# Optimization experiments

Measured on AMD Instinct MI355X. Metric: run time of the kernel, lower is better.

## Reference

```python
import jax, jax.numpy as jnp
import numpy as np

N = 20000
E = 320000
NEG_SLOPE = 0.2
LN_EPS = 1e-5


def gat_conv(x, W, a_src, a_dst, b, src, dst, heads, ch, concat):
    # x: [N, F_in]; W: [F_in, H*C]; a_src/a_dst: [H, C]; b: [H*C] or [C]
    xl = (x @ W).reshape(N, heads, ch)                      # [N,H,C]
    alpha_src = jnp.sum(xl * a_src, axis=-1)                # [N,H]
    alpha_dst = jnp.sum(xl * a_dst, axis=-1)                # [N,H]
    e = alpha_src[src] + alpha_dst[dst]                     # [E',H]
    e = jax.nn.leaky_relu(e, NEG_SLOPE)
    # segment softmax over incoming edges of each dst node
    m = jax.ops.segment_max(e, dst, num_segments=N)         # [N,H]
    m = jnp.where(jnp.isfinite(m), m, 0.0)
    ex = jnp.exp(e - m[dst])
    denom = jax.ops.segment_sum(ex, dst, num_segments=N)    # [N,H]
    alpha = ex / (denom[dst] + 1e-16)                       # [E',H]
    msg = alpha[:, :, None] * xl[src]                       # [E',H,C]
    out = jax.ops.segment_sum(msg, dst, num_segments=N)     # [N,H,C]
    if concat:
        return out.reshape(N, heads * ch) + b
    return out.mean(axis=1) + b


def layer_norm(x, g, b):
    mu = jnp.mean(x, axis=-1, keepdims=True)
    var = jnp.mean(jnp.square(x - mu), axis=-1, keepdims=True)
    return (x - mu) * jax.lax.rsqrt(var + LN_EPS) * g + b


def setup_inputs() -> dict:
    key = jax.random.key(0)
    ks = jax.random.split(key, 24)
    d = {}
    d["x"] = jax.random.normal(ks[0], (N, 50), dtype=jnp.float32)
    d["edge_index"] = jax.random.randint(ks[1], (2, E), 0, N, dtype=jnp.int64)

    def glorot(k, shape):
        fan = shape[0] + shape[-1]
        return jax.random.normal(k, shape, dtype=jnp.float32) * np.sqrt(2.0 / fan)

    # conv1: 50 -> 256, heads=4, concat
    d["W1"] = glorot(ks[2], (50, 4 * 256))
    d["a_src1"] = glorot(ks[3], (4, 256))
    d["a_dst1"] = glorot(ks[4], (4, 256))
    d["b1"] = jnp.zeros((4 * 256,), jnp.float32)
    # conv2: 1024 -> 256, heads=4, concat
    d["W2"] = glorot(ks[5], (1024, 4 * 256))
    d["a_src2"] = glorot(ks[6], (4, 256))
    d["a_dst2"] = glorot(ks[7], (4, 256))
    d["b2"] = jnp.zeros((4 * 256,), jnp.float32)
    # conv3: 1024 -> 121, heads=6, concat=False
    d["W3"] = glorot(ks[8], (1024, 6 * 121))
    d["a_src3"] = glorot(ks[9], (6, 121))
    d["a_dst3"] = glorot(ks[10], (6, 121))
    d["b3"] = jnp.zeros((121,), jnp.float32)
    # skips
    d["skipW1"] = glorot(ks[11], (50, 1024))
    d["skipb1"] = jnp.zeros((1024,), jnp.float32)
    d["skipW2"] = glorot(ks[12], (1024, 1024))
    d["skipb2"] = jnp.zeros((1024,), jnp.float32)
    # layer norms
    d["g1"] = jnp.ones((1024,), jnp.float32)
    d["beta1"] = jnp.zeros((1024,), jnp.float32)
    d["g2"] = jnp.ones((1024,), jnp.float32)
    d["beta2"] = jnp.zeros((1024,), jnp.float32)
    return d


def reference(x, edge_index, W1, a_src1, a_dst1, b1, W2, a_src2, a_dst2, b2,
              W3, a_src3, a_dst3, b3, skipW1, skipb1, skipW2, skipb2,
              g1, beta1, g2, beta2):
    # add self loops (PyG GATConv default)
    loop = jnp.arange(N, dtype=edge_index.dtype)
    src = jnp.concatenate([edge_index[0], loop])
    dst = jnp.concatenate([edge_index[1], loop])

    h = gat_conv(x, W1, a_src1, a_dst1, b1, src, dst, 4, 256, True)
    h = jax.nn.elu(layer_norm(h + (x @ skipW1 + skipb1), g1, beta1))
    h2 = gat_conv(h, W2, a_src2, a_dst2, b2, src, dst, 4, 256, True)
    h2 = jax.nn.elu(layer_norm(h2 + (h @ skipW2 + skipb2), g2, beta2))
    out = gat_conv(h2, W3, a_src3, a_dst3, b3, src, dst, 6, 121, False)
    return out
```

## Files before the change

### kernel.cpp

```cpp
#include <hip/hip_runtime.h>
#include <hip/hip_bf16.h>
#include <math.h>

typedef __attribute__((ext_vector_type(8))) __bf16 bf16x8;
typedef __attribute__((ext_vector_type(4))) float f32x4;

#define MPAD 20224
#define SSZ ((size_t)MPAD * 128)

#if __has_builtin(__builtin_amdgcn_global_load_lds)
#define GLD16(g, l)                                                                      \
    __builtin_amdgcn_global_load_lds(                                                    \
        (const __attribute__((address_space(1))) unsigned int*)(g),                      \
        (__attribute__((address_space(3))) unsigned int*)(l), 16, 0, 0)
#else
#define GLD16(g, l) (*(bf16x8*)(l) = *(const bf16x8*)(g))
#endif

#define BAR() asm volatile("s_barrier" ::: "memory")
#define WAITVM(N) asm volatile("s_waitcnt vmcnt(" #N ")" ::: "memory")


#define STAGE_T(t_)                                                                      \
    do {                                                                                 \
        __bf16* Ld = lds + (((t_) & 3) * 16384);                                         \
        const __bf16* Ga = Abase + (t_) * 32;                                            \
        const __bf16* Gb = Bbase + (t_) * 32;                                            \
        GLD16(Ga, Ld + tt * 8);                                                          \
        GLD16(Ga + (size_t)128 * K_, Ld + (tt + 512) * 8);                               \
        GLD16(Gb, Ld + 8192 + tt * 8);                                                   \
        GLD16(Gb + (size_t)128 * K_, Ld + 8192 + (tt + 512) * 8);                        \
    } while (0)

#define LOAD_FRAGS(t_)                                                                   \
    {                                                                                    \
        const __bf16* Ar = lds + (((t_) & 3) * 16384) + aoff;                            \
        const __bf16* Br = lds + (((t_) & 3) * 16384) + 8192 + boff;                     \
        _Pragma("unroll") for (int i = 0; i < 8; i++)                                    \
            af[i] = *(const bf16x8*)(Ar + i * 512);                                      \
        _Pragma("unroll") for (int j = 0; j < 4; j++)                                    \
            bf[j] = *(const bf16x8*)(Br + j * 512);                                      \
    }

#define MFMA_ALL()                                                                       \
    __builtin_amdgcn_s_setprio(1);                                                       \
    _Pragma("unroll") for (int i = 0; i < 8; i++)                                        \
        _Pragma("unroll") for (int j = 0; j < 4; j++)                                    \
            acc[i][j] = __builtin_amdgcn_mfma_f32_16x16x32_bf16(af[i], bf[j],            \
                                                                acc[i][j], 0, 0, 0);     \
    __builtin_amdgcn_s_setprio(0);

#define GEMM256_BODY(A, Bt, K_, STORE)                                                   \
    __shared__ __align__(16) __bf16 lds[65536];                                          \
    const int tt = threadIdx.x;                                                          \
    const int lane = tt & 63;                                                            \
    const int wid = tt >> 6;                                                             \
    const int wr = wid >> 2;                                           \
    const int wc = wid & 3;                                         \
     \
    const int nwg = gridDim.x * gridDim.y;                                               \
    const int wg0 = blockIdx.y * gridDim.x + blockIdx.x;                                 \
    const int qq = nwg >> 3, rr = nwg & 7, xcd = wg0 & 7, oo = wg0 >> 3;                 \
    const int swz = (xcd < rr ? xcd * (qq + 1) : rr * (qq + 1) + (xcd - rr) * qq) + oo;  \
    const int bm = (swz / gridDim.x) * 256;                                              \
    const int bn = (swz % gridDim.x) * 256;                                              \
    const int m16 = lane & 15;                                                           \
    const int c4 = lane >> 4;                                                            \
    const int NT = K_ >> 5;                                                              \
    const int ttp = tt ^ (((tt >> 5) & 1) << 1);          \
    const int srow = ttp >> 2;                                                           \
    const int sch = (ttp & 3) << 3;                                                      \
    const __bf16* Abase = A + (size_t)(bm + srow) * K_ + sch;                            \
    const __bf16* Bbase = Bt + (size_t)(bn + srow) * K_ + sch;                           \
    const int fsw = ((m16 >> 3) & 1) << 4;                                               \
    const int aoff = (((wr * 128 + m16) * 32) + c4 * 8) ^ fsw;                           \
    const int boff = (((wc * 64 + m16) * 32) + c4 * 8) ^ fsw;                            \
    f32x4 acc[8][4];                                                                     \
    _Pragma("unroll") for (int i = 0; i < 8; i++)                                        \
        _Pragma("unroll") for (int j = 0; j < 4; j++)                                    \
            acc[i][j] = (f32x4){0.f, 0.f, 0.f, 0.f};                                     \
    bf16x8 af[8], bf[4];                                                                 \
                      \
    STAGE_T(0);                                                                          \
    if (NT > 1) STAGE_T(1);                                                              \
    if (NT > 2) STAGE_T(2);                                                              \
    if (NT > 2) { WAITVM(8); } else if (NT > 1) { WAITVM(4); } else { WAITVM(0); }       \
    BAR();                                                                               \
    for (int t = 0; t < NT; t++) {                                                       \
        if (t + 3 < NT) STAGE_T(t + 3);                                                  \
        LOAD_FRAGS(t);                                                                   \
        MFMA_ALL();                                                                      \
        if (t + 1 < NT) {                                                                \
            if (t + 3 < NT) { WAITVM(8); }                                               \
            else if (t + 3 == NT) { WAITVM(4); }                                         \
            else { WAITVM(0); }                                                          \
            BAR();                                                                       \
        }                                                                                \
    }                                                                                    \
    STORE

__global__ __launch_bounds__(512, 2) void gemm256_bt(const __bf16* __restrict__ A,
                                                     const __bf16* __restrict__ Bt,
                                                     __bf16* __restrict__ C,
                                                     int M, int N_, int K_) {
    GEMM256_BODY(A, Bt, K_,
        { const int r4 = c4 << 2;
          const int rb = bm + wr * 128;
          _Pragma("unroll") for (int i = 0; i < 8; i++)
              _Pragma("unroll") for (int j = 0; j < 4; j++) {
                  int col = bn + wc * 64 + j * 16 + m16;
                  size_t sb_ = (size_t)(col >> 7) * SSZ + (col & 127);
                  _Pragma("unroll") for (int r = 0; r < 4; r++) {
                      int row = rb + i * 16 + r4 + r;
                      C[sb_ + (size_t)row * 128] = (__bf16)acc[i][j][r];
                  }
              } })
}

__global__ __launch_bounds__(512, 2) void gemm256_bt2(const __bf16* __restrict__ A,
                                                      const __bf16* __restrict__ Bt,
                                                      __bf16* __restrict__ C0,
                                                      __bf16* __restrict__ C1,
                                                      int M, int K_) {
    GEMM256_BODY(A, Bt, K_,
        { const int r4 = c4 << 2;
          const int rb = bm + wr * 128;
          _Pragma("unroll") for (int i = 0; i < 8; i++)
              _Pragma("unroll") for (int j = 0; j < 4; j++) {
                  int col = bn + wc * 64 + j * 16 + m16;
                  __bf16* Cp = (col < 1024) ? C0 : C1;
                  int c10 = col & 1023;
                  size_t sb_ = (size_t)(c10 >> 7) * SSZ + (c10 & 127);
                  _Pragma("unroll") for (int r = 0; r < 4; r++) {
                      int row = rb + i * 16 + r4 + r;
                      Cp[sb_ + (size_t)row * 128] = (__bf16)acc[i][j][r];
                  }
              } })
}

__device__ __forceinline__ void transpose_tile(const float* __restrict__ W,
                                               __bf16* __restrict__ WT,
                                               int K, int N, int Kp, int Np,
                                               int bx, int by, float* sm) {
    int tx = threadIdx.x & 31, ty = threadIdx.x >> 5;
#pragma unroll
    for (int r = ty; r < 32; r += 8) {
        int k = by * 32 + r, n = bx * 32 + tx;
        float v = 0.f;
        if (k < K && n < N) v = W[(size_t)k * N + n];
        sm[r * 33 + tx] = v;
    }
    __syncthreads();
#pragma unroll
    for (int r = ty; r < 32; r += 8) {
        int n = bx * 32 + r, k = by * 32 + tx;
        if (n < Np && k < Kp) WT[(size_t)n * Kp + k] = (__bf16)sm[tx * 33 + r];
    }
}

__device__ __forceinline__ void transpose_w3_tile(const float* __restrict__ W,
                                                  __bf16* __restrict__ WT,
                                                  int bx, int by, float* sm) {
    int tx = threadIdx.x & 31, ty = threadIdx.x >> 5;
    int r0 = bx * 32;
    int h = r0 >> 7;
    int c0 = r0 & 127;
#pragma unroll
    for (int r = ty; r < 32; r += 8) {
        int k = by * 32 + r;
        int c = c0 + tx;
        float v = 0.f;
        if (c < 121) v = W[(size_t)k * 726 + h * 121 + c];
        sm[r * 33 + tx] = v;
    }
    __syncthreads();
#pragma unroll
    for (int r = ty; r < 32; r += 8) {
        int rr = r0 + r;
        int k = by * 32 + tx;
        WT[(size_t)rr * 1024 + k] = (__bf16)sm[tx * 33 + r];
    }
}

__global__ __launch_bounds__(256) void prep_k(const float* __restrict__ x,
                                              const float* __restrict__ W1,
                                              const float* __restrict__ sW1,
                                              const float* __restrict__ W2,
                                              const float* __restrict__ sW2,
                                              const float* __restrict__ W3,
                                              __bf16* __restrict__ xp,
                                              __bf16* __restrict__ WTcat1,
                                              __bf16* __restrict__ WTcat2,
                                              __bf16* __restrict__ W3pT, int Nn) {
    __shared__ float sm[32 * 33];
    int b = blockIdx.x;
    if (b < 5056) {
        int i = b * 256 + threadIdx.x;
        int n = i >> 6, c = i & 63;
        float v = 0.f;
        if (n < Nn && c < 50) v = x[n * 50 + c];
        xp[(size_t)n * 64 + c] = (__bf16)v;
    } else if (b < 5120) {
        int i = b - 5056; transpose_tile(W1, WTcat1, 50, 1024, 64, 1024, i % 32, i / 32, sm);
    } else if (b < 5184) {
        int i = b - 5120; transpose_tile(sW1, WTcat1 + 1024 * 64, 50, 1024, 64, 1024, i % 32, i / 32, sm);
    } else if (b < 6208) {
        int i = b - 5184; transpose_tile(W2, WTcat2, 1024, 1024, 1024, 1024, i % 32, i / 32, sm);
    } else if (b < 7232) {
        int i = b - 6208; transpose_tile(sW2, WTcat2 + (size_t)1024 * 1024, 1024, 1024, 1024, 1024, i % 32, i / 32, sm);
    } else {
        int i = b - 7232; transpose_w3_tile(W3, W3pT, i % 24, i / 24, sm);
    }
}

__global__ void zero_probe_k(const int* __restrict__ ei, int* __restrict__ cnt,
                             int* __restrict__ flag, int Nn) {
    int i = blockIdx.x * 256 + threadIdx.x;
    if (i < Nn) cnt[i] = 0;
    if (blockIdx.x == 0 && threadIdx.x == 0) {
        int all0 = 1;
        for (int k = 0; k < 64; k++)
            if (ei[2 * k + 1] != 0) { all0 = 0; break; }
        *flag = all0;
    }
}

__device__ __forceinline__ int load_ei(const int* ei, int idx, int is64) {
    return is64 ? ei[2 * idx] : ei[idx];
}

__global__ void hist_k(const int* __restrict__ ei, const int* __restrict__ flag,
                       int* __restrict__ cnt, int E, int Nn) {
    int e = blockIdx.x * 256 + threadIdx.x;
    if (e >= E + Nn) return;
    int is64 = *flag;
    int d = (e < E) ? load_ei(ei, E + e, is64) : (e - E);
    d = min(max(d, 0), Nn - 1);
    atomicAdd(&cnt[d], 1);
}

__global__ __launch_bounds__(1024) void scan_k(int* __restrict__ cnt, int* __restrict__ row_ptr,
                                               int Nn) {
    __shared__ int part[1024];
    int t = threadIdx.x;
    int chunk = (Nn + 1023) >> 10;
    int lo = t * chunk;
    int hi = lo + chunk; if (hi > Nn) hi = Nn; if (lo > Nn) lo = Nn;
    int s = 0;
    for (int i = lo; i < hi; i++) s += (cnt[i] + 7) & ~7;
    part[t] = s;
    __syncthreads();
    for (int off = 1; off < 1024; off <<= 1) {
        int v = (t >= off) ? part[t - off] : 0;
        __syncthreads();
        part[t] += v;
        __syncthreads();
    }
    int run = part[t] - s;
    for (int i = lo; i < hi; i++) { row_ptr[i] = run; run += (cnt[i] + 7) & ~7; }
    if (t == 1023) row_ptr[Nn] = part[1023];
    __syncthreads();
    for (int i = lo; i < hi; i++) cnt[i] = 0;
}

__global__ void fill_csr_k(const int* __restrict__ ei, const int* __restrict__ flag,
                           const int* __restrict__ row_ptr, int* __restrict__ cursor,
                           int* __restrict__ src_csr, int E, int Nn) {
    int e = blockIdx.x * 256 + threadIdx.x;
    if (e >= E + Nn) return;
    int is64 = *flag;
    int d = (e < E) ? load_ei(ei, E + e, is64) : (e - E);
    int s = (e < E) ? load_ei(ei, e, is64) : (e - E);
    d = min(max(d, 0), Nn - 1);
    s = min(max(s, 0), Nn - 1);
    int slot = row_ptr[d] + atomicAdd(&cursor[d], 1);
    src_csr[slot] = s;
}

__global__ void alpha_k(const __bf16* __restrict__ XL, int sph, const float* __restrict__ a_src,
                        const float* __restrict__ a_dst, float* __restrict__ asrc,
                        float* __restrict__ adst, int Nn, int H, int C) {
    int gw = (blockIdx.x * 256 + threadIdx.x) >> 6;
    int lane = threadIdx.x & 63;
    if (gw >= Nn * H) return;
    int n = gw / H, h = gw - n * H;
    const float* as = a_src + h * C;
    const float* ad = a_dst + h * C;
    float s = 0.f, d = 0.f;
    for (int c = lane; c < C; c += 64) {
        float v = (float)XL[(size_t)(h * sph + (c >> 7)) * SSZ + (size_t)n * 128 + (c & 127)];
        s += v * as[c];
        d += v * ad[c];
    }
#pragma unroll
    for (int off = 32; off; off >>= 1) {
        s += __shfl_down(s, off);
        d += __shfl_down(d, off);
    }
    if (lane == 0) { asrc[n * H + h] = s; adst[n * H + h] = d; }
}

__global__ void attn_k(const int* __restrict__ row_ptr, const int* __restrict__ deg,
                       const int* __restrict__ src_csr,
                       const float* __restrict__ asrc, const float* __restrict__ adst,
                       float* __restrict__ wt, int Nn, int H, int Ecap) {
    int gw = (blockIdx.x * 256 + threadIdx.x) >> 6;
    int lane = threadIdx.x & 63;
    if (gw >= Nn) return;
    int n = gw;
    int base = row_ptr[n], dg = deg[n];
    if (dg <= 64) {
        bool v = lane < dg;
        int src = v ? src_csr[base + lane] : 0;
        for (int h = 0; h < H; h++) {
            float ad = adst[n * H + h];
            float e = -1e30f;
            if (v) {
                e = asrc[src * H + h] + ad;
                e = e > 0.f ? e : 0.2f * e;
            }
            float m = e;
#pragma unroll
            for (int off = 1; off < 64; off <<= 1) m = fmaxf(m, __shfl_xor(m, off));
            float ex = v ? __expf(e - m) : 0.f;
            float sum = ex;
#pragma unroll
            for (int off = 1; off < 64; off <<= 1) sum += __shfl_xor(sum, off);
            if (v) wt[(size_t)h * Ecap + base + lane] = ex / (sum + 1e-16f);
        }
        return;
    }
    for (int h = 0; h < H; h++) {
        float ad = adst[n * H + h];
        float m = -1e30f;
        for (int s = lane; s < dg; s += 64) {
            float e = asrc[src_csr[base + s] * H + h] + ad;
            e = e > 0.f ? e : 0.2f * e;
            m = fmaxf(m, e);
        }
#pragma unroll
        for (int off = 1; off < 64; off <<= 1) m = fmaxf(m, __shfl_xor(m, off));
        float sum = 0.f;
        for (int s = lane; s < dg; s += 64) {
            float e = asrc[src_csr[base + s] * H + h] + ad;
            e = e > 0.f ? e : 0.2f * e;
            sum += __expf(e - m);
        }
#pragma unroll
        for (int off = 1; off < 64; off <<= 1) sum += __shfl_xor(sum, off);
        float inv = 1.f / (sum + 1e-16f);
        float* wrow = wt + (size_t)h * Ecap;
        for (int s = lane; s < dg; s += 64) {
            float e = asrc[src_csr[base + s] * H + h] + ad;
            e = e > 0.f ? e : 0.2f * e;
            wrow[base + s] = __expf(e - m) * inv;
        }
    }
}

__global__ __launch_bounds__(256) void agg_skip8(const __bf16* __restrict__ XL,
                                                 const float* __restrict__ wt,
                                                 const int* __restrict__ row_ptr,
                                                 const int* __restrict__ src_csr,
                                                 const float* __restrict__ bias,
                                                 const float* __restrict__ sb,
                                                 __bf16* __restrict__ SK, int Nn, int Ecap) {
    const int cc = blockIdx.y;
    const int n = blockIdx.x * 4 + (threadIdx.x >> 6);
    const int lane = threadIdx.x & 63;
    if (n >= Nn) return;
    const int g = lane >> 4;
    const int p = lane & 15;
    const int col = cc * 128 + p * 8;
    const float* wrow = wt + (size_t)(cc >> 1) * Ecap;
    const __bf16* XLc = XL + (size_t)cc * SSZ + p * 8;
    const int base = row_ptr[n], end = row_ptr[n + 1];

    float acc[8];
#pragma unroll
    for (int j = 0; j < 8; j++) acc[j] = 0.f;

    for (int e = base; e < end; e += 8) {
        int2 si = *(const int2*)(src_csr + e + 2 * g);
        float2 wv = *(const float2*)(wrow + e + 2 * g);
        bf16x8 xa = *(const bf16x8*)(XLc + (size_t)si.x * 128);
        bf16x8 xb = *(const bf16x8*)(XLc + (size_t)si.y * 128);
#pragma unroll
        for (int j = 0; j < 8; j++) acc[j] += wv.x * (float)xa[j] + wv.y * (float)xb[j];
    }
#pragma unroll
    for (int j = 0; j < 8; j++) {
        acc[j] += __shfl_xor(acc[j], 16);
        acc[j] += __shfl_xor(acc[j], 32);
    }
    if (lane < 16) {
        size_t o = (size_t)cc * SSZ + (size_t)n * 128 + p * 8;
        bf16x8 sk = *(const bf16x8*)(SK + o);
        bf16x8 res;
#pragma unroll
        for (int j = 0; j < 8; j++)
            res[j] = (__bf16)(acc[j] + bias[col + j] + sb[col + j] + (float)sk[j]);
        *(bf16x8*)(SK + o) = res;
    }
}

__global__ __launch_bounds__(256) void agg_mean8(const __bf16* __restrict__ XL,
                                                 const float* __restrict__ wt,
                                                 const int* __restrict__ row_ptr,
                                                 const int* __restrict__ src_csr,
                                                 __bf16* __restrict__ part, int Nn, int Ecap) {
    const int cc = blockIdx.y;
    const int n = blockIdx.x * 4 + (threadIdx.x >> 6);
    const int lane = threadIdx.x & 63;
    if (n >= Nn) return;
    const int g = lane >> 4;
    const int p = lane & 15;
    const int col = cc * 128 + p * 8;
    const float* wrow = wt + (size_t)cc * Ecap;
    const __bf16* XLc = XL + (size_t)cc * SSZ + p * 8;
    const int base = row_ptr[n], end = row_ptr[n + 1];

    float acc[8];
#pragma unroll
    for (int j = 0; j < 8; j++) acc[j] = 0.f;

    for (int e = base; e < end; e += 8) {
        int2 si = *(const int2*)(src_csr + e + 2 * g);
        float2 wv = *(const float2*)(wrow + e + 2 * g);
        bf16x8 xa = *(const bf16x8*)(XLc + (size_t)si.x * 128);
        bf16x8 xb = *(const bf16x8*)(XLc + (size_t)si.y * 128);
#pragma unroll
        for (int j = 0; j < 8; j++) acc[j] += wv.x * (float)xa[j] + wv.y * (float)xb[j];
    }
#pragma unroll
    for (int j = 0; j < 8; j++) {
        acc[j] += __shfl_xor(acc[j], 16);
        acc[j] += __shfl_xor(acc[j], 32);
    }
    if (lane < 16) {
        size_t o = (size_t)n * 768 + col;
        bf16x8 res;
#pragma unroll
        for (int j = 0; j < 8; j++) res[j] = (__bf16)acc[j];
        *(bf16x8*)(part + o) = res;
    }
}

__global__ __launch_bounds__(128) void reduce_mean_k(const __bf16* __restrict__ part,
                                                     const float* __restrict__ b3,
                                                     float* __restrict__ out, int Nn) {
    int n = blockIdx.x;
    int t = threadIdx.x;
    if (t >= 121) return;
    const __bf16* row = part + (size_t)n * 768;
    float s = 0.f;
#pragma unroll
    for (int h = 0; h < 6; h++) s += (float)row[h * 128 + t];
    out[(size_t)n * 121 + t] = s * (1.f / 6.f) + b3[t];
}

__global__ __launch_bounds__(256) void ln_elu_k(const __bf16* __restrict__ in,
                                                const float* __restrict__ g,
                                                const float* __restrict__ be,
                                                __bf16* __restrict__ out, int rows_real) {
    const int D = 1024;
    int n = blockIdx.x;
    int t = threadIdx.x;
    size_t ro = (size_t)n * D;
    if (n >= rows_real) {
#pragma unroll
        for (int j = 0; j < 4; j++) out[ro + t + 256 * j] = (__bf16)0.f;
        return;
    }
    float v[4];
    float s = 0.f, q = 0.f;
#pragma unroll
    for (int j = 0; j < 4; j++) {
        int c = t + 256 * j;
        float a = (float)in[(size_t)(c >> 7) * SSZ + (size_t)n * 128 + (c & 127)];
        v[j] = a;
        s += a;
        q += a * a;
    }
#pragma unroll
    for (int off = 32; off; off >>= 1) {
        s += __shfl_down(s, off);
        q += __shfl_down(q, off);
    }
    __shared__ float rs[8];
    int wid = t >> 6;
    if ((t & 63) == 0) { rs[wid] = s; rs[wid + 4] = q; }
    __syncthreads();
    s = rs[0] + rs[1] + rs[2] + rs[3];
    q = rs[4] + rs[5] + rs[6] + rs[7];
    float mu = s * (1.f / 1024.f);
    float var = q * (1.f / 1024.f) - mu * mu;
    float inv = rsqrtf(fmaxf(var, 0.f) + 1e-5f);
#pragma unroll
    for (int j = 0; j < 4; j++) {
        int c = t + 256 * j;
        float y = (v[j] - mu) * inv * g[c] + be[c];
        y = y > 0.f ? y : expm1f(y);
        out[ro + c] = (__bf16)y;
    }
}

extern "C" void kernel_launch(void* const* d_in, const int* in_sizes, int n_in,
                              void* d_out, int out_size, void* d_ws, size_t ws_size,
                              hipStream_t stream) {
    const float* x   = (const float*)d_in[0];
    const int*   ei  = (const int*)d_in[1];
    const float* W1  = (const float*)d_in[2];
    const float* as1 = (const float*)d_in[3];
    const float* ad1 = (const float*)d_in[4];
    const float* b1  = (const float*)d_in[5];
    const float* W2  = (const float*)d_in[6];
    const float* as2 = (const float*)d_in[7];
    const float* ad2 = (const float*)d_in[8];
    const float* b2  = (const float*)d_in[9];
    const float* W3  = (const float*)d_in[10];
    const float* as3 = (const float*)d_in[11];
    const float* ad3 = (const float*)d_in[12];
    const float* b3  = (const float*)d_in[13];
    const float* sW1 = (const float*)d_in[14];
    const float* sb1 = (const float*)d_in[15];
    const float* sW2 = (const float*)d_in[16];
    const float* sb2 = (const float*)d_in[17];
    const float* g1  = (const float*)d_in[18];
    const float* be1 = (const float*)d_in[19];
    const float* g2  = (const float*)d_in[20];
    const float* be2 = (const float*)d_in[21];
    float* out = (float*)d_out;

    const int Nn = 20000;
    const int E = in_sizes[1] / 2;
    const int E2 = E + Nn;
    const int Ecap = E2 + 8 * Nn;
    const int Mpad = MPAD;

    char* p = (char*)d_ws;
    auto alloc = [&](size_t bytes) {
        char* r = p;
        p += (bytes + 255) & ~(size_t)255;
        return r;
    };
    __bf16* WTcat1 = (__bf16*)alloc((size_t)2048 * 64 * 2);
    __bf16* WTcat2 = (__bf16*)alloc((size_t)2048 * 1024 * 2);
    __bf16* W3pT   = (__bf16*)alloc((size_t)768 * 1024 * 2);
    __bf16* xp     = (__bf16*)alloc((size_t)Mpad * 64 * 2);
    __bf16* XL     = (__bf16*)alloc((size_t)Mpad * 1024 * 2);
    __bf16* SK     = (__bf16*)alloc((size_t)Mpad * 1024 * 2);
    __bf16* H1     = (__bf16*)alloc((size_t)Mpad * 1024 * 2);
    float*  asrcb  = (float*)alloc((size_t)Nn * 6 * 4);
    float*  adstb  = (float*)alloc((size_t)Nn * 6 * 4);
    float*  wbuf   = (float*)alloc((size_t)6 * Ecap * 4);
    int*    rowp   = (int*)alloc((size_t)(Nn + 1) * 4);
    int*    cnt    = (int*)alloc((size_t)Nn * 4);
    int*    scsr   = (int*)alloc((size_t)Ecap * 4);
    int*    eiflag = (int*)alloc(256);
    __bf16* part   = SK;
    (void)ws_size; (void)n_in; (void)out_size;

    prep_k<<<8000, 256, 0, stream>>>(x, W1, sW1, W2, sW2, W3, xp, WTcat1, WTcat2, W3pT, Nn);

    zero_probe_k<<<(Nn + 255) / 256, 256, 0, stream>>>(ei, cnt, eiflag, Nn);
    hist_k<<<(E2 + 255) / 256, 256, 0, stream>>>(ei, eiflag, cnt, E, Nn);
    scan_k<<<1, 1024, 0, stream>>>(cnt, rowp, Nn);
    (void)hipMemsetAsync(scsr, 0, (size_t)Ecap * 4, stream);
    (void)hipMemsetAsync(wbuf, 0, (size_t)6 * Ecap * 4, stream);
    fill_csr_k<<<(E2 + 255) / 256, 256, 0, stream>>>(ei, eiflag, rowp, cnt, scsr, E, Nn);

    gemm256_bt2<<<dim3(8, Mpad / 256), 512, 0, stream>>>(xp, WTcat1, XL, SK, Mpad, 64);
    alpha_k<<<(Nn * 4 * 64) / 256, 256, 0, stream>>>(XL, 2, as1, ad1, asrcb, adstb, Nn, 4, 256);
    attn_k<<<(Nn + 3) / 4, 256, 0, stream>>>(rowp, cnt, scsr, asrcb, adstb, wbuf, Nn, 4, Ecap);
    agg_skip8<<<dim3((Nn + 3) / 4, 8), 256, 0, stream>>>(XL, wbuf, rowp, scsr, b1, sb1, SK, Nn, Ecap);
    ln_elu_k<<<Mpad, 256, 0, stream>>>(SK, g1, be1, H1, Nn);

    gemm256_bt2<<<dim3(8, Mpad / 256), 512, 0, stream>>>(H1, WTcat2, XL, SK, Mpad, 1024);
    alpha_k<<<(Nn * 4 * 64) / 256, 256, 0, stream>>>(XL, 2, as2, ad2, asrcb, adstb, Nn, 4, 256);
    attn_k<<<(Nn + 3) / 4, 256, 0, stream>>>(rowp, cnt, scsr, asrcb, adstb, wbuf, Nn, 4, Ecap);
    agg_skip8<<<dim3((Nn + 3) / 4, 8), 256, 0, stream>>>(XL, wbuf, rowp, scsr, b2, sb2, SK, Nn, Ecap);
    ln_elu_k<<<Mpad, 256, 0, stream>>>(SK, g2, be2, H1, Nn);

    gemm256_bt<<<dim3(3, Mpad / 256), 512, 0, stream>>>(H1, W3pT, XL, Mpad, 768, 1024);
    alpha_k<<<(Nn * 6 * 64) / 256, 256, 0, stream>>>(XL, 1, as3, ad3, asrcb, adstb, Nn, 6, 121);
    attn_k<<<(Nn + 3) / 4, 256, 0, stream>>>(rowp, cnt, scsr, asrcb, adstb, wbuf, Nn, 6, Ecap);
    agg_mean8<<<dim3((Nn + 3) / 4, 6), 256, 0, stream>>>(XL, wbuf, rowp, scsr, part, Nn, Ecap);
    reduce_mean_k<<<Nn, 128, 0, stream>>>(part, b3, out, Nn);
}
```

Baseline: 750.4 us.

## Software-pipeline LDS fragment loads for next K tile under current MFMAs

The bf16 GEMM main loop now reads the next tile's A/B fragments from LDS interleaved with the current tile's MFMA instructions, instead of loading all fragments before the MFMAs. To keep this correct, the prologue and per-iteration vmcnt waits are tightened so tile t+1 is resident before tile t's MFMAs begin. This hides LDS read latency behind matrix math. The cost is more register pressure and somewhat earlier waits on the global-to-LDS copies.

```diff
diff --git a/kernel.cpp b/kernel.cpp
--- a/kernel.cpp
+++ b/kernel.cpp
@@ -42,13 +42,38 @@
             bf[j] = *(const bf16x8*)(Br + j * 512);                                      \
     }
 
-#define MFMA_ALL()                                                                       \
-    __builtin_amdgcn_s_setprio(1);                                                       \
-    _Pragma("unroll") for (int i = 0; i < 8; i++)                                        \
-        _Pragma("unroll") for (int j = 0; j < 4; j++)                                    \
-            acc[i][j] = __builtin_amdgcn_mfma_f32_16x16x32_bf16(af[i], bf[j],            \
-                                                                acc[i][j], 0, 0, 0);     \
-    __builtin_amdgcn_s_setprio(0);
+#define MFMA1(i_, j_)                                                                    \
+    acc[i_][j_] = __builtin_amdgcn_mfma_f32_16x16x32_bf16(af[i_], bf[j_],                \
+                                                          acc[i_][j_], 0, 0, 0);
+
+#define MFMA_TILE_PRE(t_)                                                                \
+    {                                                                                    \
+        const __bf16* ArN = lds + ((((t_) + 1) & 3) * 16384) + aoff;                     \
+        const __bf16* BrN = lds + ((((t_) + 1) & 3) * 16384) + 8192 + boff;              \
+        __builtin_amdgcn_s_setprio(1);                                                   \
+        _Pragma("unroll") for (int i = 0; i < 7; i++) {                                  \
+            _Pragma("unroll") for (int j = 0; j < 4; j++) { MFMA1(i, j) }                \
+            af[i] = *(const bf16x8*)(ArN + i * 512);                                     \
+        }                                                                                \
+        MFMA1(7, 0)                                                                      \
+        bf[0] = *(const bf16x8*)(BrN + 0 * 512);                                         \
+        MFMA1(7, 1)                                                                      \
+        bf[1] = *(const bf16x8*)(BrN + 1 * 512);                                         \
+        MFMA1(7, 2)                                                                      \
+        bf[2] = *(const bf16x8*)(BrN + 2 * 512);                                         \
+        MFMA1(7, 3)                                                                      \
+        bf[3] = *(const bf16x8*)(BrN + 3 * 512);                                         \
+        af[7] = *(const bf16x8*)(ArN + 7 * 512);                                         \
+        __builtin_amdgcn_s_setprio(0);                                                   \
+    }
+
+#define MFMA_TILE_LAST()                                                                 \
+    {                                                                                    \
+        __builtin_amdgcn_s_setprio(1);                                                   \
+        _Pragma("unroll") for (int i = 0; i < 8; i++)                                    \
+            _Pragma("unroll") for (int j = 0; j < 4; j++) { MFMA1(i, j) }                \
+        __builtin_amdgcn_s_setprio(0);                                                   \
+    }
 
 #define GEMM256_BODY(A, Bt, K_, STORE)                                                   \
     __shared__ __align__(16) __bf16 lds[65536];                                          \
@@ -80,22 +105,18 @@
         _Pragma("unroll") for (int j = 0; j < 4; j++)                                    \
             acc[i][j] = (f32x4){0.f, 0.f, 0.f, 0.f};                                     \
     bf16x8 af[8], bf[4];                                                                 \
-                      \
+          \
     STAGE_T(0);                                                                          \
     if (NT > 1) STAGE_T(1);                                                              \
     if (NT > 2) STAGE_T(2);                                                              \
-    if (NT > 2) { WAITVM(8); } else if (NT > 1) { WAITVM(4); } else { WAITVM(0); }       \
+    if (NT > 2) { WAITVM(4); } else { WAITVM(0); }                                       \
     BAR();                                                                               \
+    LOAD_FRAGS(0);                                                                       \
     for (int t = 0; t < NT; t++) {                                                       \
         if (t + 3 < NT) STAGE_T(t + 3);                                                  \
-        LOAD_FRAGS(t);                                                                   \
-        MFMA_ALL();                                                                      \
-        if (t + 1 < NT) {                                                                \
-            if (t + 3 < NT) { WAITVM(8); }                                               \
-            else if (t + 3 == NT) { WAITVM(4); }                                         \
-            else { WAITVM(0); }                                                          \
-            BAR();                                                                       \
-        }                                                                                \
+        if (t + 1 < NT) { MFMA_TILE_PRE(t); } else { MFMA_TILE_LAST(); }                 \
+        if (t + 3 < NT) { WAITVM(4); BAR(); }                                            \
+        else if (t + 3 == NT) { WAITVM(0); BAR(); }                                      \
     }                                                                                    \
     STORE
 
```

Measured after the change: 1.717 ms. 2.29x slower.

## Fuse attention-logit dot products into GEMM epilogue and vectorize LayerNorm-ELU

Applied to the files above, without the earlier changes.

Removes the separate alpha_k kernel by computing each head's src/dst attention logits inside the GEMM epilogue. Each wave does partial dot products over its 64 columns, reduces them across lanes with xor-shuffles, and atomically adds them into buffers zeroed by new memsets. This avoids re-reading the bf16 XL tensor from memory, at the cost of extra epilogue work, atomics and memsets. Separately, ln_elu_k now handles two rows per block with 8-wide vector loads and stores.

```diff
diff --git a/kernel.cpp b/kernel.cpp
--- a/kernel.cpp
+++ b/kernel.cpp
@@ -50,7 +50,7 @@
                                                                 acc[i][j], 0, 0, 0);     \
     __builtin_amdgcn_s_setprio(0);
 
-#define GEMM256_BODY(A, Bt, K_, STORE)                                                   \
+#define GEMM256_BODY(A, Bt, K_, ...)                                                     \
     __shared__ __align__(16) __bf16 lds[65536];                                          \
     const int tt = threadIdx.x;                                                          \
     const int lane = tt & 63;                                                            \
@@ -97,12 +97,16 @@
             BAR();                                                                       \
         }                                                                                \
     }                                                                                    \
-    STORE
+    __VA_ARGS__
 
 __global__ __launch_bounds__(512, 2) void gemm256_bt(const __bf16* __restrict__ A,
                                                      const __bf16* __restrict__ Bt,
                                                      __bf16* __restrict__ C,
-                                                     int M, int N_, int K_) {
+                                                     int M, int N_, int K_,
+                                                     const float* __restrict__ a_src,
+                                                     const float* __restrict__ a_dst,
+                                                     float* __restrict__ asrc,
+                                                     float* __restrict__ adst, int Nn_) {
     GEMM256_BODY(A, Bt, K_,
         { const int r4 = c4 << 2;
           const int rb = bm + wr * 128;
@@ -114,14 +118,43 @@
                       int row = rb + i * 16 + r4 + r;
                       C[sb_ + (size_t)row * 128] = (__bf16)acc[i][j][r];
                   }
-              } })
+              }
+          { const int h = (bn + wc * 64) >> 7;
+            const int cw = (wc * 64) & 127;
+            float asv[4];
+            float adv[4];
+            _Pragma("unroll") for (int j = 0; j < 4; j++) {
+                int cp = cw + j * 16 + m16;
+                asv[j] = (cp < 121) ? a_src[h * 121 + cp] : 0.f;
+                adv[j] = (cp < 121) ? a_dst[h * 121 + cp] : 0.f;
+            }
+            _Pragma("unroll") for (int i = 0; i < 8; i++)
+                _Pragma("unroll") for (int r = 0; r < 4; r++) {
+                    int row = rb + i * 16 + r4 + r;
+                    float s = acc[i][0][r] * asv[0] + acc[i][1][r] * asv[1] +
+                              acc[i][2][r] * asv[2] + acc[i][3][r] * asv[3];
+                    float d = acc[i][0][r] * adv[0] + acc[i][1][r] * adv[1] +
+                              acc[i][2][r] * adv[2] + acc[i][3][r] * adv[3];
+                    _Pragma("unroll") for (int off = 1; off < 16; off <<= 1) {
+                        s += __shfl_xor(s, off);
+                        d += __shfl_xor(d, off);
+                    }
+                    if (m16 == 0 && row < Nn_) {
+                        atomicAdd(&asrc[row * 6 + h], s);
+                        atomicAdd(&adst[row * 6 + h], d);
+                    }
+                } } })
 }
 
 __global__ __launch_bounds__(512, 2) void gemm256_bt2(const __bf16* __restrict__ A,
                                                       const __bf16* __restrict__ Bt,
                                                       __bf16* __restrict__ C0,
                                                       __bf16* __restrict__ C1,
-                                                      int M, int K_) {
+                                                      int M, int K_,
+                                                      const float* __restrict__ a_src,
+                                                      const float* __restrict__ a_dst,
+                                                      float* __restrict__ asrc,
+                                                      float* __restrict__ adst, int Nn_) {
     GEMM256_BODY(A, Bt, K_,
         { const int r4 = c4 << 2;
           const int rb = bm + wr * 128;
@@ -135,7 +168,33 @@
                       int row = rb + i * 16 + r4 + r;
                       Cp[sb_ + (size_t)row * 128] = (__bf16)acc[i][j][r];
                   }
-              } })
+              }
+          if (bn < 1024) {
+              const int h = bn >> 8;
+              float asv[4];
+              float adv[4];
+              _Pragma("unroll") for (int j = 0; j < 4; j++) {
+                  int cp = wc * 64 + j * 16 + m16;
+                  asv[j] = a_src[h * 256 + cp];
+                  adv[j] = a_dst[h * 256 + cp];
+              }
+              _Pragma("unroll") for (int i = 0; i < 8; i++)
+                  _Pragma("unroll") for (int r = 0; r < 4; r++) {
+                      int row = rb + i * 16 + r4 + r;
+                      float s = acc[i][0][r] * asv[0] + acc[i][1][r] * asv[1] +
+                                acc[i][2][r] * asv[2] + acc[i][3][r] * asv[3];
+                      float d = acc[i][0][r] * adv[0] + acc[i][1][r] * adv[1] +
+                                acc[i][2][r] * adv[2] + acc[i][3][r] * adv[3];
+                      _Pragma("unroll") for (int off = 1; off < 16; off <<= 1) {
+                          s += __shfl_xor(s, off);
+                          d += __shfl_xor(d, off);
+                      }
+                      if (m16 == 0 && row < Nn_) {
+                          atomicAdd(&asrc[row * 4 + h], s);
+                          atomicAdd(&adst[row * 4 + h], d);
+                      }
+                  }
+          } })
 }
 
 __device__ __forceinline__ void transpose_tile(const float* __restrict__ W,
@@ -277,29 +336,6 @@
     src_csr[slot] = s;
 }
 
-__global__ void alpha_k(const __bf16* __restrict__ XL, int sph, const float* __restrict__ a_src,
-                        const float* __restrict__ a_dst, float* __restrict__ asrc,
-                        float* __restrict__ adst, int Nn, int H, int C) {
-    int gw = (blockIdx.x * 256 + threadIdx.x) >> 6;
-    int lane = threadIdx.x & 63;
-    if (gw >= Nn * H) return;
-    int n = gw / H, h = gw - n * H;
-    const float* as = a_src + h * C;
-    const float* ad = a_dst + h * C;
-    float s = 0.f, d = 0.f;
-    for (int c = lane; c < C; c += 64) {
-        float v = (float)XL[(size_t)(h * sph + (c >> 7)) * SSZ + (size_t)n * 128 + (c & 127)];
-        s += v * as[c];
-        d += v * ad[c];
-    }
-#pragma unroll
-    for (int off = 32; off; off >>= 1) {
-        s += __shfl_down(s, off);
-        d += __shfl_down(d, off);
-    }
-    if (lane == 0) { asrc[n * H + h] = s; adst[n * H + h] = d; }
-}
-
 __global__ void attn_k(const int* __restrict__ row_ptr, const int* __restrict__ deg,
                        const int* __restrict__ src_csr,
                        const float* __restrict__ asrc, const float* __restrict__ adst,
@@ -463,46 +499,54 @@
                                                 const float* __restrict__ g,
                                                 const float* __restrict__ be,
                                                 __bf16* __restrict__ out, int rows_real) {
-    const int D = 1024;
-    int n = blockIdx.x;
-    int t = threadIdx.x;
-    size_t ro = (size_t)n * D;
-    if (n >= rows_real) {
-#pragma unroll
-        for (int j = 0; j < 4; j++) out[ro + t + 256 * j] = (__bf16)0.f;
-        return;
-    }
-    float v[4];
+    const int half = threadIdx.x >> 7;
+    const int t = threadIdx.x & 127;
+    const int n = blockIdx.x * 2 + half;
+    const size_t ro = (size_t)n * 1024 + t * 8;
+    __shared__ float rs[8];
+    bf16x8 v8;
+    float v[8];
     float s = 0.f, q = 0.f;
-#pragma unroll
-    for (int j = 0; j < 4; j++) {
-        int c = t + 256 * j;
-        float a = (float)in[(size_t)(c >> 7) * SSZ + (size_t)n * 128 + (c & 127)];
-        v[j] = a;
-        s += a;
-        q += a * a;
+    const bool live = (n < rows_real);
+    if (live) {
+        v8 = *(const bf16x8*)(in + (size_t)(t >> 4) * SSZ + (size_t)n * 128 + (t & 15) * 8);
+#pragma unroll
+        for (int j = 0; j < 8; j++) {
+            v[j] = (float)v8[j];
+            s += v[j];
+            q += v[j] * v[j];
+        }
     }
 #pragma unroll
     for (int off = 32; off; off >>= 1) {
         s += __shfl_down(s, off);
         q += __shfl_down(q, off);
     }
-    __shared__ float rs[8];
-    int wid = t >> 6;
-    if ((t & 63) == 0) { rs[wid] = s; rs[wid + 4] = q; }
+    int wid = threadIdx.x >> 6;
+    if ((threadIdx.x & 63) == 0) { rs[wid] = s; rs[wid + 4] = q; }
     __syncthreads();
-    s = rs[0] + rs[1] + rs[2] + rs[3];
-    q = rs[4] + rs[5] + rs[6] + rs[7];
+    if (!live) {
+        bf16x8 z;
+#pragma unroll
+        for (int j = 0; j < 8; j++) z[j] = (__bf16)0.f;
+        *(bf16x8*)(out + ro) = z;
+        return;
+    }
+    int w0 = half * 2;
+    s = rs[w0] + rs[w0 + 1];
+    q = rs[w0 + 4] + rs[w0 + 5];
     float mu = s * (1.f / 1024.f);
     float var = q * (1.f / 1024.f) - mu * mu;
     float inv = rsqrtf(fmaxf(var, 0.f) + 1e-5f);
-#pragma unroll
-    for (int j = 0; j < 4; j++) {
-        int c = t + 256 * j;
+    bf16x8 o8;
+#pragma unroll
+    for (int j = 0; j < 8; j++) {
+        int c = t * 8 + j;
         float y = (v[j] - mu) * inv * g[c] + be[c];
         y = y > 0.f ? y : expm1f(y);
-        out[ro + c] = (__bf16)y;
-    }
+        o8[j] = (__bf16)y;
+    }
+    *(bf16x8*)(out + ro) = o8;
 }
 
 extern "C" void kernel_launch(void* const* d_in, const int* in_sizes, int n_in,
@@ -570,20 +614,26 @@
     (void)hipMemsetAsync(wbuf, 0, (size_t)6 * Ecap * 4, stream);
     fill_csr_k<<<(E2 + 255) / 256, 256, 0, stream>>>(ei, eiflag, rowp, cnt, scsr, E, Nn);
 
-    gemm256_bt2<<<dim3(8, Mpad / 256), 512, 0, stream>>>(xp, WTcat1, XL, SK, Mpad, 64);
-    alpha_k<<<(Nn * 4 * 64) / 256, 256, 0, stream>>>(XL, 2, as1, ad1, asrcb, adstb, Nn, 4, 256);
+    (void)hipMemsetAsync(asrcb, 0, (size_t)Nn * 6 * 4, stream);
+    (void)hipMemsetAsync(adstb, 0, (size_t)Nn * 6 * 4, stream);
+    gemm256_bt2<<<dim3(8, Mpad / 256), 512, 0, stream>>>(xp, WTcat1, XL, SK, Mpad, 64,
+                                                         as1, ad1, asrcb, adstb, Nn);
     attn_k<<<(Nn + 3) / 4, 256, 0, stream>>>(rowp, cnt, scsr, asrcb, adstb, wbuf, Nn, 4, Ecap);
     agg_skip8<<<dim3((Nn + 3) / 4, 8), 256, 0, stream>>>(XL, wbuf, rowp, scsr, b1, sb1, SK, Nn, Ecap);
-    ln_elu_k<<<Mpad, 256, 0, stream>>>(SK, g1, be1, H1, Nn);
-
-    gemm256_bt2<<<dim3(8, Mpad / 256), 512, 0, stream>>>(H1, WTcat2, XL, SK, Mpad, 1024);
-    alpha_k<<<(Nn * 4 * 64) / 256, 256, 0, stream>>>(XL, 2, as2, ad2, asrcb, adstb, Nn, 4, 256);
+    ln_elu_k<<<Mpad / 2, 256, 0, stream>>>(SK, g1, be1, H1, Nn);
+
+    (void)hipMemsetAsync(asrcb, 0, (size_t)Nn * 6 * 4, stream);
+    (void)hipMemsetAsync(adstb, 0, (size_t)Nn * 6 * 4, stream);
+    gemm256_bt2<<<dim3(8, Mpad / 256), 512, 0, stream>>>(H1, WTcat2, XL, SK, Mpad, 1024,
+                                                         as2, ad2, asrcb, adstb, Nn);
     attn_k<<<(Nn + 3) / 4, 256, 0, stream>>>(rowp, cnt, scsr, asrcb, adstb, wbuf, Nn, 4, Ecap);
     agg_skip8<<<dim3((Nn + 3) / 4, 8), 256, 0, stream>>>(XL, wbuf, rowp, scsr, b2, sb2, SK, Nn, Ecap);
-    ln_elu_k<<<Mpad, 256, 0, stream>>>(SK, g2, be2, H1, Nn);
-
-    gemm256_bt<<<dim3(3, Mpad / 256), 512, 0, stream>>>(H1, W3pT, XL, Mpad, 768, 1024);
-    alpha_k<<<(Nn * 6 * 64) / 256, 256, 0, stream>>>(XL, 1, as3, ad3, asrcb, adstb, Nn, 6, 121);
+    ln_elu_k<<<Mpad / 2, 256, 0, stream>>>(SK, g2, be2, H1, Nn);
+
+    (void)hipMemsetAsync(asrcb, 0, (size_t)Nn * 6 * 4, stream);
+    (void)hipMemsetAsync(adstb, 0, (size_t)Nn * 6 * 4, stream);
+    gemm256_bt<<<dim3(3, Mpad / 256), 512, 0, stream>>>(H1, W3pT, XL, Mpad, 768, 1024,
+                                                        as3, ad3, asrcb, adstb, Nn);
     attn_k<<<(Nn + 3) / 4, 256, 0, stream>>>(rowp, cnt, scsr, asrcb, adstb, wbuf, Nn, 6, Ecap);
     agg_mean8<<<dim3((Nn + 3) / 4, 6), 256, 0, stream>>>(XL, wbuf, rowp, scsr, part, Nn, Ecap);
     reduce_mean_k<<<Nn, 128, 0, stream>>>(part, b3, out, Nn);
```

Result: slower. 929.1 us (+23.8%).

## Remap aggregation grids for XCD locality and vectorize LayerNorm-ELU rows

Applied to the files above, without the earlier changes.

The aggregation kernels now use a 1D grid. In agg_skip8 the eight column chunks of a node group land on consecutive blocks, and agg_mean8 applies an XCD-aware swizzle, both meant to improve L2 reuse of the gathered source rows. The LayerNorm+ELU kernel now processes two rows per block with 16-byte bf16x8 loads and stores instead of scalar accesses, halving the block count. The agg_mean8 swizzle hard-codes 3750 and 5000, so it is only correct for N=20000 with 6 heads.

```diff
diff --git a/kernel.cpp b/kernel.cpp
--- a/kernel.cpp
+++ b/kernel.cpp
@@ -50,7 +50,7 @@
                                                                 acc[i][j], 0, 0, 0);     \
     __builtin_amdgcn_s_setprio(0);
 
-#define GEMM256_BODY(A, Bt, K_, STORE)                                                   \
+#define GEMM256_BODY(A, Bt, K_, ...)                                                     \
     __shared__ __align__(16) __bf16 lds[65536];                                          \
     const int tt = threadIdx.x;                                                          \
     const int lane = tt & 63;                                                            \
@@ -97,7 +97,7 @@
             BAR();                                                                       \
         }                                                                                \
     }                                                                                    \
-    STORE
+    __VA_ARGS__
 
 __global__ __launch_bounds__(512, 2) void gemm256_bt(const __bf16* __restrict__ A,
                                                      const __bf16* __restrict__ Bt,
@@ -365,8 +365,9 @@
                                                  const float* __restrict__ bias,
                                                  const float* __restrict__ sb,
                                                  __bf16* __restrict__ SK, int Nn, int Ecap) {
-    const int cc = blockIdx.y;
-    const int n = blockIdx.x * 4 + (threadIdx.x >> 6);
+    const int bid = blockIdx.x;
+    const int cc = bid & 7;
+    const int n = (bid >> 3) * 4 + (threadIdx.x >> 6);
     const int lane = threadIdx.x & 63;
     if (n >= Nn) return;
     const int g = lane >> 4;
@@ -409,8 +410,11 @@
                                                  const int* __restrict__ row_ptr,
                                                  const int* __restrict__ src_csr,
                                                  __bf16* __restrict__ part, int Nn, int Ecap) {
-    const int cc = blockIdx.y;
-    const int n = blockIdx.x * 4 + (threadIdx.x >> 6);
+    const int bid = blockIdx.x;
+    const int swz = (bid & 7) * 3750 + (bid >> 3);
+    const int cc = swz / 5000;
+    const int nb = swz - cc * 5000;
+    const int n = nb * 4 + (threadIdx.x >> 6);
     const int lane = threadIdx.x & 63;
     if (n >= Nn) return;
     const int g = lane >> 4;
@@ -463,46 +467,54 @@
                                                 const float* __restrict__ g,
                                                 const float* __restrict__ be,
                                                 __bf16* __restrict__ out, int rows_real) {
-    const int D = 1024;
-    int n = blockIdx.x;
-    int t = threadIdx.x;
-    size_t ro = (size_t)n * D;
-    if (n >= rows_real) {
-#pragma unroll
-        for (int j = 0; j < 4; j++) out[ro + t + 256 * j] = (__bf16)0.f;
-        return;
-    }
-    float v[4];
+    const int half = threadIdx.x >> 7;
+    const int t = threadIdx.x & 127;
+    const int n = blockIdx.x * 2 + half;
+    const size_t ro = (size_t)n * 1024 + t * 8;
+    __shared__ float rs[8];
+    bf16x8 v8;
+    float v[8];
     float s = 0.f, q = 0.f;
-#pragma unroll
-    for (int j = 0; j < 4; j++) {
-        int c = t + 256 * j;
-        float a = (float)in[(size_t)(c >> 7) * SSZ + (size_t)n * 128 + (c & 127)];
-        v[j] = a;
-        s += a;
-        q += a * a;
+    const bool live = (n < rows_real);
+    if (live) {
+        v8 = *(const bf16x8*)(in + (size_t)(t >> 4) * SSZ + (size_t)n * 128 + (t & 15) * 8);
+#pragma unroll
+        for (int j = 0; j < 8; j++) {
+            v[j] = (float)v8[j];
+            s += v[j];
+            q += v[j] * v[j];
+        }
     }
 #pragma unroll
     for (int off = 32; off; off >>= 1) {
         s += __shfl_down(s, off);
         q += __shfl_down(q, off);
     }
-    __shared__ float rs[8];
-    int wid = t >> 6;
-    if ((t & 63) == 0) { rs[wid] = s; rs[wid + 4] = q; }
+    int wid = threadIdx.x >> 6;
+    if ((threadIdx.x & 63) == 0) { rs[wid] = s; rs[wid + 4] = q; }
     __syncthreads();
-    s = rs[0] + rs[1] + rs[2] + rs[3];
-    q = rs[4] + rs[5] + rs[6] + rs[7];
+    if (!live) {
+        bf16x8 z;
+#pragma unroll
+        for (int j = 0; j < 8; j++) z[j] = (__bf16)0.f;
+        *(bf16x8*)(out + ro) = z;
+        return;
+    }
+    int w0 = half * 2;
+    s = rs[w0] + rs[w0 + 1];
+    q = rs[w0 + 4] + rs[w0 + 5];
     float mu = s * (1.f / 1024.f);
     float var = q * (1.f / 1024.f) - mu * mu;
     float inv = rsqrtf(fmaxf(var, 0.f) + 1e-5f);
-#pragma unroll
-    for (int j = 0; j < 4; j++) {
-        int c = t + 256 * j;
+    bf16x8 o8;
+#pragma unroll
+    for (int j = 0; j < 8; j++) {
+        int c = t * 8 + j;
         float y = (v[j] - mu) * inv * g[c] + be[c];
         y = y > 0.f ? y : expm1f(y);
-        out[ro + c] = (__bf16)y;
-    }
+        o8[j] = (__bf16)y;
+    }
+    *(bf16x8*)(out + ro) = o8;
 }
 
 extern "C" void kernel_launch(void* const* d_in, const int* in_sizes, int n_in,
@@ -573,18 +585,18 @@
     gemm256_bt2<<<dim3(8, Mpad / 256), 512, 0, stream>>>(xp, WTcat1, XL, SK, Mpad, 64);
     alpha_k<<<(Nn * 4 * 64) / 256, 256, 0, stream>>>(XL, 2, as1, ad1, asrcb, adstb, Nn, 4, 256);
     attn_k<<<(Nn + 3) / 4, 256, 0, stream>>>(rowp, cnt, scsr, asrcb, adstb, wbuf, Nn, 4, Ecap);
-    agg_skip8<<<dim3((Nn + 3) / 4, 8), 256, 0, stream>>>(XL, wbuf, rowp, scsr, b1, sb1, SK, Nn, Ecap);
-    ln_elu_k<<<Mpad, 256, 0, stream>>>(SK, g1, be1, H1, Nn);
+    agg_skip8<<<((Nn + 3) / 4) * 8, 256, 0, stream>>>(XL, wbuf, rowp, scsr, b1, sb1, SK, Nn, Ecap);
+    ln_elu_k<<<Mpad / 2, 256, 0, stream>>>(SK, g1, be1, H1, Nn);
 
     gemm256_bt2<<<dim3(8, Mpad / 256), 512, 0, stream>>>(H1, WTcat2, XL, SK, Mpad, 1024);
     alpha_k<<<(Nn * 4 * 64) / 256, 256, 0, stream>>>(XL, 2, as2, ad2, asrcb, adstb, Nn, 4, 256);
     attn_k<<<(Nn + 3) / 4, 256, 0, stream>>>(rowp, cnt, scsr, asrcb, adstb, wbuf, Nn, 4, Ecap);
-    agg_skip8<<<dim3((Nn + 3) / 4, 8), 256, 0, stream>>>(XL, wbuf, rowp, scsr, b2, sb2, SK, Nn, Ecap);
-    ln_elu_k<<<Mpad, 256, 0, stream>>>(SK, g2, be2, H1, Nn);
+    agg_skip8<<<((Nn + 3) / 4) * 8, 256, 0, stream>>>(XL, wbuf, rowp, scsr, b2, sb2, SK, Nn, Ecap);
+    ln_elu_k<<<Mpad / 2, 256, 0, stream>>>(SK, g2, be2, H1, Nn);
 
     gemm256_bt<<<dim3(3, Mpad / 256), 512, 0, stream>>>(H1, W3pT, XL, Mpad, 768, 1024);
     alpha_k<<<(Nn * 6 * 64) / 256, 256, 0, stream>>>(XL, 1, as3, ad3, asrcb, adstb, Nn, 6, 121);
     attn_k<<<(Nn + 3) / 4, 256, 0, stream>>>(rowp, cnt, scsr, asrcb, adstb, wbuf, Nn, 6, Ecap);
-    agg_mean8<<<dim3((Nn + 3) / 4, 6), 256, 0, stream>>>(XL, wbuf, rowp, scsr, part, Nn, Ecap);
+    agg_mean8<<<((Nn + 3) / 4) * 6, 256, 0, stream>>>(XL, wbuf, rowp, scsr, part, Nn, Ecap);
     reduce_mean_k<<<Nn, 128, 0, stream>>>(part, b3, out, Nn);
 }
```

Measured after the change: 845.5 us. +12.7%, slower.
